# Performance work log

Hardware: AMD Instinct MI355X
Metric: run time of the kernel (lower is better)

The kernel has to match this reference:

```python
import jax, jax.numpy as jnp
import numpy as np


def setup_inputs() -> dict:
    key = jax.random.key(0)
    k1, k2, k3 = jax.random.split(key, 3)
    B, S, D, L = 64, 2048, 512, 4
    x = jax.random.normal(k1, (B, S, D), dtype=jnp.float32)
    Wh = jax.random.normal(k2, (L, D, D), dtype=jnp.float32)
    Uh = jax.random.normal(k3, (L, D, D), dtype=jnp.float32)
    b = jnp.zeros((L, D), dtype=jnp.float32)
    return {"x": x, "Wh": Wh, "Uh": Uh, "b": b}


def reference(x, Wh, Uh, b):
    # x: [B, S, D]; Wh/Uh: [L, D, D]; b: [L, D]
    B, S, D = x.shape
    L = Wh.shape[0]

    def step(h, x_t):
        # h: [L, B, D] hidden states per layer; x_t: [B, D]
        inp = x_t
        new_hs = []
        for l in range(L):  # small fixed layer count
            hn = jnp.tanh(inp @ Wh[l] + h[l] @ Uh[l] + b[l])
            new_hs.append(hn)
            inp = hn
        return jnp.stack(new_hs, axis=0), inp

    h0 = jnp.zeros((L, B, D), dtype=x.dtype)
    xs = jnp.transpose(x, (1, 0, 2))  # [S, B, D] for scan over time
    _, outs = jax.lax.scan(step, h0, xs)  # outs: [S, B, D]
    return jnp.transpose(outs, (1, 0, 2))  # [B, S, D]
```

## Files before the change

### kernel.cpp

```cpp
#include <hip/hip_runtime.h>
#include <hip/hip_cooperative_groups.h>

namespace cg = cooperative_groups;

constexpr int kB = 64, kS = 2048, kD = 512, kL = 4;
constexpr int kR = 8;
constexpr int RING_F = kR * kL * kB * kD;
constexpr int ZBUF_F = kB * kD;
constexpr int CNT_N  = kL * 8 * kS;
constexpr size_t NEED_WS = (size_t)(RING_F + ZBUF_F + CNT_N) * 4 + 4096;

__device__ __forceinline__ float tanh_ref(float x0) {
#pragma clang fp contract(off)
  const float kMax = 7.99881172180175781f;
  float xc = fminf(fmaxf(x0, -kMax), kMax);
  float x2 = xc * xc;
  float p = -2.76076847742355e-16f;
  p = fmaf(x2, p, 2.00018790482477e-13f);
  p = fmaf(x2, p, -8.60467152213735e-11f);
  p = fmaf(x2, p, 5.12229709037114e-08f);
  p = fmaf(x2, p, 1.48572235717979e-05f);
  p = fmaf(x2, p, 6.37261928875436e-04f);
  p = fmaf(x2, p, 4.89352455891786e-03f);
  float num = xc * p;
  float q = 1.19825839466702e-06f;
  q = fmaf(x2, q, 1.18534705686654e-04f);
  q = fmaf(x2, q, 2.26843463243900e-03f);
  q = fmaf(x2, q, 4.89352518554385e-03f);
  float r = num / q;
  return (fabsf(x0) < 0.0004f) ? x0 : r;
}

__global__ void prep_zero(float* __restrict__ zbuf, unsigned* __restrict__ cnt) {
  const int gid = blockIdx.x * blockDim.x + threadIdx.x;
  for (int i = gid; i < ZBUF_F; i += gridDim.x * blockDim.x) zbuf[i] = 0.f;
  for (int i = gid; i < CNT_N; i += gridDim.x * blockDim.x) cnt[i] = 0u;
}

__device__ __forceinline__ unsigned cnt_ld(const unsigned* p) {
  return __hip_atomic_load(p, __ATOMIC_RELAXED, __HIP_MEMORY_SCOPE_AGENT);
}

__device__ __forceinline__ float lane_bcast(float v, int kk) {
  return __uint_as_float(__builtin_amdgcn_readlane(__float_as_uint(v), kk));
}

__global__ __launch_bounds__(256, 1) void rnn_pipe3(
    const float* __restrict__ x, const float* __restrict__ Wh,
    const float* __restrict__ Uh, const float* __restrict__ bias,
    float* __restrict__ out, float* __restrict__ ring,
    float* __restrict__ zbuf, unsigned* __restrict__ cnt) {
  const int tid = threadIdx.x, bid = blockIdx.x;
  const int l  = bid >> 6;
  const int bg = (bid >> 3) & 7;
  const int jg = bid & 7;
  const int jl = tid & 63;
  const int bq = tid >> 6;
  const int j  = jg * 64 + jl;
  const int b0 = bg * 8 + bq * 2;
  const int b1 = b0 + 1;

  const float* Wcol = Wh + (long)l * kD * kD + j;
  const float* Ucol = Uh + (long)l * kD * kD + j;
  const float bv = bias[l * kD + j];

  const unsigned* cSibling = cnt + ((long)l * 8 + bg) * kS;
  const unsigned* cBelow   = (l > 0) ? cnt + ((long)(l - 1) * 8 + bg) * kS : nullptr;
  const unsigned* cAbove   = (l < kL - 1) ? cnt + ((long)(l + 1) * 8 + bg) * kS : nullptr;
  unsigned* cMine = cnt + ((long)l * 8 + bg) * kS;

  for (int t = 0; t < kS; ++t) {
    if (tid == 0) {
      if (t > 0)             while (cnt_ld(&cSibling[t - 1]) < 8u) __builtin_amdgcn_s_sleep(1);
      if (l > 0)             while (cnt_ld(&cBelow[t]) < 8u)       __builtin_amdgcn_s_sleep(1);
      if (cAbove && t >= kR) while (cnt_ld(&cAbove[t - kR]) < 8u)  __builtin_amdgcn_s_sleep(1);
      __threadfence();
    }
    __syncthreads();

    const int slot  = t & (kR - 1);
    const int slotP = (t - 1) & (kR - 1);
    const float* i0row, *i1row;
    if (l == 0) {
      i0row = x + ((long)b0 * kS + t) * kD;
      i1row = x + ((long)b1 * kS + t) * kD;
    } else {
      i0row = ring + (((long)slot * kL + (l - 1)) * kB + b0) * (long)kD;
      i1row = i0row + kD;
    }
    const float* h0row = (t == 0)
        ? zbuf + (long)b0 * kD
        : ring + (((long)slotP * kL + l) * kB + b0) * (long)kD;
    const float* h1row = h0row + kD;

    float dw0, dw1, du0, du1;
    {
#pragma clang fp contract(off)
      dw0 = 0.f; dw1 = 0.f; du0 = 0.f; du1 = 0.f;
      float ni0 = i0row[jl], ni1 = i1row[jl];
      float nh0 = h0row[jl], nh1 = h1row[jl];
      for (int ch = 0; ch < 8; ++ch) {
        const float vi0 = ni0, vi1 = ni1, vh0 = nh0, vh1 = nh1;
        if (ch < 7) {
          const int nb = (ch + 1) * 64 + jl;
          ni0 = i0row[nb]; ni1 = i1row[nb];
          nh0 = h0row[nb]; nh1 = h1row[nb];
        }
        const int base = ch * 64;
#pragma unroll
        for (int kk = 0; kk < 64; ++kk) {
          const float wv = Wcol[(long)(base + kk) * kD];
          const float uv = Ucol[(long)(base + kk) * kD];
          const float ai0 = lane_bcast(vi0, kk);
          const float ai1 = lane_bcast(vi1, kk);
          const float ah0 = lane_bcast(vh0, kk);
          const float ah1 = lane_bcast(vh1, kk);
          dw0 = fmaf(ai0, wv, dw0);
          dw1 = fmaf(ai1, wv, dw1);
          du0 = fmaf(ah0, uv, du0);
          du1 = fmaf(ah1, uv, du1);
        }
      }
    }
    float z0, z1;
    {
#pragma clang fp contract(off)
      z0 = (dw0 + du0) + bv;
      z1 = (dw1 + du1) + bv;
    }
    const float h0 = tanh_ref(z0);
    const float h1 = tanh_ref(z1);

    float* ho = ring + (((long)slot * kL + l) * kB) * (long)kD;
    ho[(long)b0 * kD + j] = h0;
    ho[(long)b1 * kD + j] = h1;
    if (l == kL - 1) {
      out[((long)b0 * kS + t) * kD + j] = h0;
      out[((long)b1 * kS + t) * kD + j] = h1;
    }

    __syncthreads();
    if (tid == 0) {
      __threadfence();
      atomicAdd(&cMine[t], 1u);
    }
  }
}

__global__ __launch_bounds__(256, 1) void rnn_full(
    const float* __restrict__ x, const float* __restrict__ Wh,
    const float* __restrict__ Uh, const float* __restrict__ bias,
    float* __restrict__ out, float* __restrict__ ws) {
  cg::grid_group grid = cg::this_grid();
  float* Hbuf = ws;
  const int tid = threadIdx.x, bid = blockIdx.x;
  const int l = bid >> 6;
  const int bg = (bid >> 3) & 7;
  const int jg = bid & 7;
  const int jl = tid & 63;
  const int bq = tid >> 6;
  const int j = jg * 64 + jl;
  const int b0 = bg * 8 + bq * 2;
  __shared__ float iS[8][512];
  __shared__ float hS[8][512];
  for (int i = bid * 256 + tid; i < 2 * kL * kB * kD; i += 256 * 256) Hbuf[i] = 0.f;
  grid.sync();
  const float* Wcol = Wh + (long)l * kD * kD + j;
  const float* Ucol = Uh + (long)l * kD * kD + j;
  const float bv = bias[l * kD + j];
  for (int w = 0; w < kS + kL - 1; ++w) {
    const int t = w - l;
    if (t >= 0 && t < kS) {
      const int cur = w & 1, prv = cur ^ 1;
      const float* hbase = Hbuf + (((long)prv * kL + l) * kB + bg * 8) * (long)kD;
      const float* ibase = (l == 0) ? nullptr
          : Hbuf + (((long)prv * kL + (l - 1)) * kB + bg * 8) * (long)kD;
      for (int i = tid; i < 8 * 128; i += 256) {
        const int rr = i >> 7, q4 = (i & 127) * 4;
        const float* isrc = (l == 0)
            ? (x + ((long)(bg * 8 + rr) * kS + t) * kD + q4)
            : (ibase + (long)rr * kD + q4);
        *(float4*)&iS[rr][q4] = *(const float4*)isrc;
        *(float4*)&hS[rr][q4] = *(const float4*)(hbase + (long)rr * kD + q4);
      }
      __syncthreads();
      const int r0 = bq * 2, r1 = r0 + 1;
      float dw0, dw1, du0, du1;
      {
#pragma clang fp contract(off)
        dw0 = 0.f; dw1 = 0.f; du0 = 0.f; du1 = 0.f;
#pragma unroll 4
        for (int k = 0; k < 512; ++k) {
          const float wv = Wcol[(long)k * kD];
          const float uv = Ucol[(long)k * kD];
          dw0 = fmaf(iS[r0][k], wv, dw0);
          dw1 = fmaf(iS[r1][k], wv, dw1);
          du0 = fmaf(hS[r0][k], uv, du0);
          du1 = fmaf(hS[r1][k], uv, du1);
        }
      }
      float z0, z1;
      {
#pragma clang fp contract(off)
        z0 = (dw0 + du0) + bv;
        z1 = (dw1 + du1) + bv;
      }
      const float h0 = tanh_ref(z0);
      const float h1 = tanh_ref(z1);
      float* ho = Hbuf + (((long)cur * kL + l) * kB) * (long)kD;
      ho[(long)b0 * kD + j] = h0;
      ho[(long)(b0 + 1) * kD + j] = h1;
      if (l == kL - 1) {
        out[((long)b0 * kS + t) * kD + j] = h0;
        out[((long)(b0 + 1) * kS + t) * kD + j] = h1;
      }
    }
    grid.sync();
  }
}

extern "C" void kernel_launch(void* const* d_in, const int* in_sizes, int n_in,
                              void* d_out, int out_size, void* d_ws, size_t ws_size,
                              hipStream_t stream) {
  const float* x    = (const float*)d_in[0];
  const float* Wh   = (const float*)d_in[1];
  const float* Uh   = (const float*)d_in[2];
  const float* bias = (const float*)d_in[3];
  float* out = (float*)d_out;
  float* ws  = (float*)d_ws;

  if (ws_size >= NEED_WS) {
    float* ring = ws;
    float* zbuf = ws + RING_F;
    unsigned* cnt = (unsigned*)(zbuf + ZBUF_F);

    prep_zero<<<128, 256, 0, stream>>>(zbuf, cnt);

    void* args[] = {(void*)&x, (void*)&Wh, (void*)&Uh, (void*)&bias,
                    (void*)&out, (void*)&ring, (void*)&zbuf, (void*)&cnt};
    hipLaunchCooperativeKernel((void*)rnn_pipe3, dim3(256), dim3(256), args, 0,
                               stream);
  } else {
    void* args[] = {(void*)&x, (void*)&Wh, (void*)&Uh, (void*)&bias,
                    (void*)&out, (void*)&ws};
    hipLaunchCooperativeKernel((void*)rnn_full, dim3(256), dim3(256), args, 0,
                               stream);
  }
}
```

Measured before the change: 48.86 ms.

## Interleave W and U into packed float2 and double-buffer weight loads

```diff
diff --git a/kernel.cpp b/kernel.cpp
--- a/kernel.cpp
+++ b/kernel.cpp
@@ -1,14 +1,13 @@
 #include <hip/hip_runtime.h>
-#include <hip/hip_cooperative_groups.h>
-
-namespace cg = cooperative_groups;
 
 constexpr int kB = 64, kS = 2048, kD = 512, kL = 4;
 constexpr int kR = 8;
 constexpr int RING_F = kR * kL * kB * kD;
 constexpr int ZBUF_F = kB * kD;
 constexpr int CNT_N  = kL * 8 * kS;
-constexpr size_t NEED_WS = (size_t)(RING_F + ZBUF_F + CNT_N) * 4 + 4096;
+constexpr long PACK_F2 = (long)kL * kD * kD;
+constexpr size_t NEED_BASE = (size_t)(RING_F + ZBUF_F + CNT_N) * 4;
+constexpr size_t NEED_PACK = NEED_BASE + (size_t)PACK_F2 * 8 + 4096;
 
 __device__ __forceinline__ float tanh_ref(float x0) {
 #pragma clang fp contract(off)
@@ -37,12 +36,142 @@
   for (int i = gid; i < CNT_N; i += gridDim.x * blockDim.x) cnt[i] = 0u;
 }
 
+__global__ void pack_wu(const float* __restrict__ W, const float* __restrict__ U,
+                        float2* __restrict__ pk) {
+  const long gid = (long)blockIdx.x * blockDim.x + threadIdx.x;
+  for (long i = gid; i < PACK_F2; i += (long)gridDim.x * blockDim.x)
+    pk[i] = make_float2(W[i], U[i]);
+}
+
 __device__ __forceinline__ unsigned cnt_ld(const unsigned* p) {
   return __hip_atomic_load(p, __ATOMIC_RELAXED, __HIP_MEMORY_SCOPE_AGENT);
 }
 
 __device__ __forceinline__ float lane_bcast(float v, int kk) {
   return __uint_as_float(__builtin_amdgcn_readlane(__float_as_uint(v), kk));
+}
+
+__device__ __forceinline__ void loadw16(float2 (&buf)[16],
+                                        const float2* __restrict__ pkc, int g) {
+#pragma unroll
+  for (int q = 0; q < 16; ++q) buf[q] = pkc[(long)(g * 16 + q) * kD];
+}
+
+__device__ __forceinline__ void consume16(const float2 (&buf)[16], int kloc,
+                                          float vi0, float vi1, float vh0, float vh1,
+                                          float& dw0, float& dw1,
+                                          float& du0, float& du1) {
+#pragma clang fp contract(off)
+#pragma unroll
+  for (int q = 0; q < 16; ++q) {
+    const int kk = kloc + q;
+    const float ai0 = lane_bcast(vi0, kk);
+    const float ai1 = lane_bcast(vi1, kk);
+    const float ah0 = lane_bcast(vh0, kk);
+    const float ah1 = lane_bcast(vh1, kk);
+    dw0 = fmaf(ai0, buf[q].x, dw0);
+    dw1 = fmaf(ai1, buf[q].x, dw1);
+    du0 = fmaf(ah0, buf[q].y, du0);
+    du1 = fmaf(ah1, buf[q].y, du1);
+  }
+}
+
+__global__ __launch_bounds__(256, 1) void rnn_pipe4(
+    const float* __restrict__ x, const float2* __restrict__ wupk,
+    const float* __restrict__ bias, float* __restrict__ out,
+    float* __restrict__ ring, float* __restrict__ zbuf,
+    unsigned* __restrict__ cnt) {
+  const int tid = threadIdx.x, bid = blockIdx.x;
+  const int l  = bid >> 6;
+  const int bg = (bid >> 3) & 7;
+  const int jg = bid & 7;
+  const int jl = tid & 63;
+  const int bq = tid >> 6;
+  const int j  = jg * 64 + jl;
+  const int b0 = bg * 8 + bq * 2;
+  const int b1 = b0 + 1;
+
+  const float2* pkc = wupk + (long)l * kD * kD + j;
+  const float bv = bias[l * kD + j];
+
+  const unsigned* cSibling = cnt + ((long)l * 8 + bg) * kS;
+  const unsigned* cBelow   = (l > 0) ? cnt + ((long)(l - 1) * 8 + bg) * kS : nullptr;
+  const unsigned* cAbove   = (l < kL - 1) ? cnt + ((long)(l + 1) * 8 + bg) * kS : nullptr;
+  unsigned* cMine = cnt + ((long)l * 8 + bg) * kS;
+
+  for (int t = 0; t < kS; ++t) {
+    if (tid == 0) {
+      if (t > 0)             while (cnt_ld(&cSibling[t - 1]) < 8u) __builtin_amdgcn_s_sleep(1);
+      if (l > 0)             while (cnt_ld(&cBelow[t]) < 8u)       __builtin_amdgcn_s_sleep(1);
+      if (cAbove && t >= kR) while (cnt_ld(&cAbove[t - kR]) < 8u)  __builtin_amdgcn_s_sleep(1);
+      __threadfence();
+    }
+    __syncthreads();
+
+    const int slot  = t & (kR - 1);
+    const int slotP = (t - 1) & (kR - 1);
+    const float* i0row, *i1row;
+    if (l == 0) {
+      i0row = x + ((long)b0 * kS + t) * kD;
+      i1row = x + ((long)b1 * kS + t) * kD;
+    } else {
+      i0row = ring + (((long)slot * kL + (l - 1)) * kB + b0) * (long)kD;
+      i1row = i0row + kD;
+    }
+    const float* h0row = (t == 0)
+        ? zbuf + (long)b0 * kD
+        : ring + (((long)slotP * kL + l) * kB + b0) * (long)kD;
+    const float* h1row = h0row + kD;
+
+    float dw0, dw1, du0, du1;
+    {
+#pragma clang fp contract(off)
+      dw0 = 0.f; dw1 = 0.f; du0 = 0.f; du1 = 0.f;
+      float2 bufA[16], bufB[16];
+      loadw16(bufA, pkc, 0);
+      float ni0 = i0row[jl], ni1 = i1row[jl];
+      float nh0 = h0row[jl], nh1 = h1row[jl];
+      float vi0 = 0.f, vi1 = 0.f, vh0 = 0.f, vh1 = 0.f;
+      for (int gp = 0; gp < 16; ++gp) {
+        const int g0 = gp * 2, g1 = g0 + 1;
+        if ((g0 & 3) == 0) {
+          vi0 = ni0; vi1 = ni1; vh0 = nh0; vh1 = nh1;
+          const int ch = g0 >> 2;
+          if (ch < 7) {
+            const int nb = (ch + 1) * 64 + jl;
+            ni0 = i0row[nb]; ni1 = i1row[nb];
+            nh0 = h0row[nb]; nh1 = h1row[nb];
+          }
+        }
+        loadw16(bufB, pkc, g1);
+        consume16(bufA, (g0 & 3) * 16, vi0, vi1, vh0, vh1, dw0, dw1, du0, du1);
+        if (g1 < 31) loadw16(bufA, pkc, g1 + 1);
+        consume16(bufB, (g1 & 3) * 16, vi0, vi1, vh0, vh1, dw0, dw1, du0, du1);
+      }
+    }
+    float z0, z1;
+    {
+#pragma clang fp contract(off)
+      z0 = (dw0 + du0) + bv;
+      z1 = (dw1 + du1) + bv;
+    }
+    const float h0 = tanh_ref(z0);
+    const float h1 = tanh_ref(z1);
+
+    float* ho = ring + (((long)slot * kL + l) * kB) * (long)kD;
+    ho[(long)b0 * kD + j] = h0;
+    ho[(long)b1 * kD + j] = h1;
+    if (l == kL - 1) {
+      out[((long)b0 * kS + t) * kD + j] = h0;
+      out[((long)b1 * kS + t) * kD + j] = h1;
+    }
+
+    __syncthreads();
+    if (tid == 0) {
+      __threadfence();
+      atomicAdd(&cMine[t], 1u);
+    }
+  }
 }
 
 __global__ __launch_bounds__(256, 1) void rnn_pipe3(
@@ -59,16 +188,13 @@
   const int j  = jg * 64 + jl;
   const int b0 = bg * 8 + bq * 2;
   const int b1 = b0 + 1;
-
   const float* Wcol = Wh + (long)l * kD * kD + j;
   const float* Ucol = Uh + (long)l * kD * kD + j;
   const float bv = bias[l * kD + j];
-
   const unsigned* cSibling = cnt + ((long)l * 8 + bg) * kS;
   const unsigned* cBelow   = (l > 0) ? cnt + ((long)(l - 1) * 8 + bg) * kS : nullptr;
   const unsigned* cAbove   = (l < kL - 1) ? cnt + ((long)(l + 1) * 8 + bg) * kS : nullptr;
   unsigned* cMine = cnt + ((long)l * 8 + bg) * kS;
-
   for (int t = 0; t < kS; ++t) {
     if (tid == 0) {
       if (t > 0)             while (cnt_ld(&cSibling[t - 1]) < 8u) __builtin_amdgcn_s_sleep(1);
@@ -77,7 +203,6 @@
       __threadfence();
     }
     __syncthreads();
-
     const int slot  = t & (kR - 1);
     const int slotP = (t - 1) & (kR - 1);
     const float* i0row, *i1row;
@@ -92,7 +217,6 @@
         ? zbuf + (long)b0 * kD
         : ring + (((long)slotP * kL + l) * kB + b0) * (long)kD;
     const float* h1row = h0row + kD;
-
     float dw0, dw1, du0, du1;
     {
 #pragma clang fp contract(off)
@@ -111,14 +235,10 @@
         for (int kk = 0; kk < 64; ++kk) {
           const float wv = Wcol[(long)(base + kk) * kD];
           const float uv = Ucol[(long)(base + kk) * kD];
-          const float ai0 = lane_bcast(vi0, kk);
-          const float ai1 = lane_bcast(vi1, kk);
-          const float ah0 = lane_bcast(vh0, kk);
-          const float ah1 = lane_bcast(vh1, kk);
-          dw0 = fmaf(ai0, wv, dw0);
-          dw1 = fmaf(ai1, wv, dw1);
-          du0 = fmaf(ah0, uv, du0);
-          du1 = fmaf(ah1, uv, du1);
+          dw0 = fmaf(lane_bcast(vi0, kk), wv, dw0);
+          dw1 = fmaf(lane_bcast(vi1, kk), wv, dw1);
+          du0 = fmaf(lane_bcast(vh0, kk), uv, du0);
+          du1 = fmaf(lane_bcast(vh1, kk), uv, du1);
         }
       }
     }
@@ -130,7 +250,6 @@
     }
     const float h0 = tanh_ref(z0);
     const float h1 = tanh_ref(z1);
-
     float* ho = ring + (((long)slot * kL + l) * kB) * (long)kD;
     ho[(long)b0 * kD + j] = h0;
     ho[(long)b1 * kD + j] = h1;
@@ -138,84 +257,11 @@
       out[((long)b0 * kS + t) * kD + j] = h0;
       out[((long)b1 * kS + t) * kD + j] = h1;
     }
-
     __syncthreads();
     if (tid == 0) {
       __threadfence();
       atomicAdd(&cMine[t], 1u);
     }
-  }
-}
-
-__global__ __launch_bounds__(256, 1) void rnn_full(
-    const float* __restrict__ x, const float* __restrict__ Wh,
-    const float* __restrict__ Uh, const float* __restrict__ bias,
-    float* __restrict__ out, float* __restrict__ ws) {
-  cg::grid_group grid = cg::this_grid();
-  float* Hbuf = ws;
-  const int tid = threadIdx.x, bid = blockIdx.x;
-  const int l = bid >> 6;
-  const int bg = (bid >> 3) & 7;
-  const int jg = bid & 7;
-  const int jl = tid & 63;
-  const int bq = tid >> 6;
-  const int j = jg * 64 + jl;
-  const int b0 = bg * 8 + bq * 2;
-  __shared__ float iS[8][512];
-  __shared__ float hS[8][512];
-  for (int i = bid * 256 + tid; i < 2 * kL * kB * kD; i += 256 * 256) Hbuf[i] = 0.f;
-  grid.sync();
-  const float* Wcol = Wh + (long)l * kD * kD + j;
-  const float* Ucol = Uh + (long)l * kD * kD + j;
-  const float bv = bias[l * kD + j];
-  for (int w = 0; w < kS + kL - 1; ++w) {
-    const int t = w - l;
-    if (t >= 0 && t < kS) {
-      const int cur = w & 1, prv = cur ^ 1;
-      const float* hbase = Hbuf + (((long)prv * kL + l) * kB + bg * 8) * (long)kD;
-      const float* ibase = (l == 0) ? nullptr
-          : Hbuf + (((long)prv * kL + (l - 1)) * kB + bg * 8) * (long)kD;
-      for (int i = tid; i < 8 * 128; i += 256) {
-        const int rr = i >> 7, q4 = (i & 127) * 4;
-        const float* isrc = (l == 0)
-            ? (x + ((long)(bg * 8 + rr) * kS + t) * kD + q4)
-            : (ibase + (long)rr * kD + q4);
-        *(float4*)&iS[rr][q4] = *(const float4*)isrc;
-        *(float4*)&hS[rr][q4] = *(const float4*)(hbase + (long)rr * kD + q4);
-      }
-      __syncthreads();
-      const int r0 = bq * 2, r1 = r0 + 1;
-      float dw0, dw1, du0, du1;
-      {
-#pragma clang fp contract(off)
-        dw0 = 0.f; dw1 = 0.f; du0 = 0.f; du1 = 0.f;
-#pragma unroll 4
-        for (int k = 0; k < 512; ++k) {
-          const float wv = Wcol[(long)k * kD];
-          const float uv = Ucol[(long)k * kD];
-          dw0 = fmaf(iS[r0][k], wv, dw0);
-          dw1 = fmaf(iS[r1][k], wv, dw1);
-          du0 = fmaf(hS[r0][k], uv, du0);
-          du1 = fmaf(hS[r1][k], uv, du1);
-        }
-      }
-      float z0, z1;
-      {
-#pragma clang fp contract(off)
-        z0 = (dw0 + du0) + bv;
-        z1 = (dw1 + du1) + bv;
-      }
-      const float h0 = tanh_ref(z0);
-      const float h1 = tanh_ref(z1);
-      float* ho = Hbuf + (((long)cur * kL + l) * kB) * (long)kD;
-      ho[(long)b0 * kD + j] = h0;
-      ho[(long)(b0 + 1) * kD + j] = h1;
-      if (l == kL - 1) {
-        out[((long)b0 * kS + t) * kD + j] = h0;
-        out[((long)(b0 + 1) * kS + t) * kD + j] = h1;
-      }
-    }
-    grid.sync();
   }
 }
 
@@ -229,21 +275,23 @@
   float* out = (float*)d_out;
   float* ws  = (float*)d_ws;
 
-  if (ws_size >= NEED_WS) {
-    float* ring = ws;
-    float* zbuf = ws + RING_F;
-    unsigned* cnt = (unsigned*)(zbuf + ZBUF_F);
-
-    prep_zero<<<128, 256, 0, stream>>>(zbuf, cnt);
-
+  float* ring = ws;
+  float* zbuf = ws + RING_F;
+  unsigned* cnt = (unsigned*)(zbuf + ZBUF_F);
+
+  prep_zero<<<128, 256, 0, stream>>>(zbuf, cnt);
+
+  if (ws_size >= NEED_PACK) {
+    float2* pk = (float2*)((char*)ws + NEED_BASE);
+    pack_wu<<<512, 256, 0, stream>>>(Wh, Uh, pk);
+    void* args[] = {(void*)&x, (void*)&pk, (void*)&bias, (void*)&out,
+                    (void*)&ring, (void*)&zbuf, (void*)&cnt};
+    hipLaunchCooperativeKernel((void*)rnn_pipe4, dim3(256), dim3(256), args, 0,
+                               stream);
+  } else {
     void* args[] = {(void*)&x, (void*)&Wh, (void*)&Uh, (void*)&bias,
                     (void*)&out, (void*)&ring, (void*)&zbuf, (void*)&cnt};
     hipLaunchCooperativeKernel((void*)rnn_pipe3, dim3(256), dim3(256), args, 0,
                                stream);
-  } else {
-    void* args[] = {(void*)&x, (void*)&Wh, (void*)&Uh, (void*)&bias,
-                    (void*)&out, (void*)&ws};
-    hipLaunchCooperativeKernel((void*)rnn_full, dim3(256), dim3(256), args, 0,
-                               stream);
-  }
-}
+  }
+}
```

After: 64.93 ms. 32.9% more time.
